# Performance work log

Measured on AMD Instinct MI355X. Metric: run time of the kernel, lower is better.

The kernel has to match this reference:

```python
import jax, jax.numpy as jnp
import numpy as np

CONF_TH = 0.9
FRACTION = 0.66
IGNORE_INDEX = 255
LAMBDA = 1.0


def setup_inputs() -> dict:
    key = jax.random.key(0)
    pred = jax.random.normal(key, (4, 19, 512, 1024), dtype=jnp.float32)
    return {"pred": pred}


def _image_mask(max_prob, pseudo, num_classes):
    # max_prob, pseudo: [N] flattened per-image. Replicates the torch per-class
    # loop: keep the top floor(count_c * FRACTION) pixels of each class c by
    # max_prob. Equivalent to: within-class descending rank < k_c.
    n = max_prob.shape[0]
    # sort by (class asc, prob desc); last key in lexsort is primary
    order = jnp.lexsort((-max_prob, pseudo))
    counts = jnp.bincount(pseudo, length=num_classes)  # [C]
    starts = jnp.concatenate([jnp.zeros(1, counts.dtype), jnp.cumsum(counts)[:-1]])
    rank_sorted = jnp.arange(n, dtype=counts.dtype) - starts[pseudo[order]]
    rank = jnp.zeros(n, counts.dtype).at[order].set(rank_sorted)
    k = jnp.floor(counts.astype(jnp.float32) * FRACTION).astype(counts.dtype)  # int(count*frac)
    mask_topk = rank < k[pseudo]
    mask_prob = max_prob > CONF_TH
    return mask_prob | mask_topk


def reference(pred):
    B, C, H, W = pred.shape
    logp = jax.nn.log_softmax(pred, axis=1)           # [B,C,H,W]
    prob = jnp.exp(logp)
    pseudo = jnp.argmax(pred, axis=1)                 # [B,H,W] (detached in torch; int here)
    max_prob = jnp.max(prob, axis=1)                  # [B,H,W]
    N = H * W
    mask = jax.vmap(lambda m, p: _image_mask(m, p, C))(
        max_prob.reshape(B, N), pseudo.reshape(B, N)
    ).reshape(B, H, W)
    target = jnp.where(mask, pseudo, IGNORE_INDEX)
    valid = target != IGNORE_INDEX
    tsafe = jnp.where(valid, target, 0)
    nll = -jnp.take_along_axis(logp, tsafe[:, None], axis=1)[:, 0]  # [B,H,W]
    # F.cross_entropy(..., reduction='none') gives 0 at ignored pixels; .mean()
    # divides by the TOTAL number of pixels (including ignored ones).
    loss = jnp.where(valid, nll, 0.0).mean() * LAMBDA
    return loss
```

## Files before the change

### kernel.cpp

```cpp
#include <hip/hip_runtime.h>
#include <math.h>

#define BB 4
#define CC 19
#define HH 512
#define WW 1024
#define NPIX (HH * WW)
#define NB 80
#define CONF_BIN 72
#define FRACTION_F 0.66f
#define ROW (CC * NB)
#define NROW (BB * CC)

#define NBLK1 512
#define BPI (NBLK1 / BB)
#define PPB (NPIX / BPI)
#define T1 512


static __device__ __forceinline__ float comp(float4 v, int j) {
    return (j == 0) ? v.x : (j == 1) ? v.y : (j == 2) ? v.z : v.w;
}

__global__ __launch_bounds__(T1, 4) void st_pass1(const float* __restrict__ pred,
                                                  int* __restrict__ cntPart,
                                                  float* __restrict__ snlPart,
                                                  float* __restrict__ out) {
    __shared__ int   hcnt[ROW];
    __shared__ float hsnl[ROW];
    int tid = threadIdx.x;
    if (blockIdx.x == 0 && tid == 0) out[0] = 0.f;
    for (int i = tid; i < ROW; i += T1) { hcnt[i] = 0; hsnl[i] = 0.f; }
    __syncthreads();

    int blk = blockIdx.x;
    int b   = blk >> 7;
    int seg = blk & (BPI - 1);
    const float* bp0 = pred + (size_t)b * CC * NPIX + (size_t)seg * PPB + tid * 4;
    const float* bp1 = bp0 + T1 * 4;

    float4 va[5], vb[5], vc[5], vd[4];
    float m[4], s[4]; int arg[4];

#define LOAD5(DST, BP, C0)                                            \
        _Pragma("unroll")                                             \
        for (int i = 0; i < 5; ++i)                                   \
            DST[i] = *(const float4*)((BP) + (size_t)(C0 + i) * NPIX);
#define LOAD4(DST, BP, C0)                                            \
        _Pragma("unroll")                                             \
        for (int i = 0; i < 4; ++i)                                   \
            DST[i] = *(const float4*)((BP) + (size_t)(C0 + i) * NPIX);
#define FENCE asm volatile("" ::: "memory")
#define INIT4(VA)                                                     \
        _Pragma("unroll")                                             \
        for (int j = 0; j < 4; ++j) { m[j] = comp(VA[0], j); s[j] = 1.f; arg[j] = 0; }
#define PROC(VA, NCH, CBASE, START)                                   \
        _Pragma("unroll")                                             \
        for (int i = START; i < NCH; ++i) {                           \
            _Pragma("unroll")                                         \
            for (int j = 0; j < 4; ++j) {                             \
                float x  = comp(VA[i], j);                            \
                float nm = fmaxf(m[j], x);                            \
                s[j] = s[j] * __expf(m[j] - nm) + __expf(x - nm);     \
                arg[j] = (x > m[j]) ? (CBASE + i) : arg[j];           \
                m[j] = nm;                                            \
            }                                                         \
        }
#define FINAL()                                                       \
        _Pragma("unroll")                                             \
        for (int j = 0; j < 4; ++j) {                                 \
            float prob = 1.f / s[j];                                  \
            float nll  = __logf(s[j]);                                \
            int bin = min((int)(prob * (float)NB), NB - 1);           \
            int idx = arg[j] * NB + bin;                              \
            atomicAdd(&hcnt[idx], 1);                                 \
            atomicAdd(&hsnl[idx], nll);                               \
        }

    LOAD5(va, bp0, 0); LOAD5(vb, bp0, 5); FENCE;
    INIT4(va)
    PROC(va, 5, 0, 1)
    LOAD5(vc, bp0, 10); FENCE;
    PROC(vb, 5, 5, 0)
    LOAD4(vd, bp0, 15); FENCE;
    PROC(vc, 5, 10, 0)
    LOAD5(va, bp1, 0); FENCE;
    PROC(vd, 4, 15, 0)
    FINAL()
    LOAD5(vb, bp1, 5); FENCE;
    INIT4(va)
    PROC(va, 5, 0, 1)
    LOAD5(vc, bp1, 10); FENCE;
    PROC(vb, 5, 5, 0)
    LOAD4(vd, bp1, 15); FENCE;
    PROC(vc, 5, 10, 0)
    PROC(vd, 4, 15, 0)
    FINAL()
#undef LOAD5
#undef LOAD4
#undef FENCE
#undef INIT4
#undef PROC
#undef FINAL
    __syncthreads();

    int*   cp = cntPart + (size_t)blk * ROW;
    float* sp = snlPart + (size_t)blk * ROW;
    for (int i = tid; i < ROW; i += T1) { cp[i] = hcnt[i]; sp[i] = hsnl[i]; }
}

__global__ __launch_bounds__(384) void st_pass2(const int* __restrict__ cntPart,
                                                const float* __restrict__ snlPart,
                                                float* __restrict__ out) {
    __shared__ int   pcnt[4][NB];
    __shared__ float psnl[4][NB];
    __shared__ int   scnt[NB];
    __shared__ float ssnl[NB];
    int r = blockIdx.x;
    int b = r / CC, c = r - b * CC;
    int tid = threadIdx.x;

    if (tid < 4 * NB) {
        int q   = tid / NB;
        int bin = tid - q * NB;
        size_t off = (size_t)(b * BPI + q * 32) * ROW + (size_t)(c * NB + bin);
        int cs0 = 0, cs1 = 0; float ss0 = 0.f, ss1 = 0.f;
        #pragma unroll 8
        for (int p = 0; p < 32; p += 2) {
            cs0 += cntPart[off + (size_t)p * ROW];
            cs1 += cntPart[off + (size_t)(p + 1) * ROW];
            ss0 += snlPart[off + (size_t)p * ROW];
            ss1 += snlPart[off + (size_t)(p + 1) * ROW];
        }
        pcnt[q][bin] = cs0 + cs1;
        psnl[q][bin] = ss0 + ss1;
    }
    __syncthreads();
    if (tid < NB) {
        scnt[tid] = (pcnt[0][tid] + pcnt[1][tid]) + (pcnt[2][tid] + pcnt[3][tid]);
        ssnl[tid] = (psnl[0][tid] + psnl[1][tid]) + (psnl[2][tid] + psnl[3][tid]);
    }
    __syncthreads();

    if (tid == 0) {
        int count = 0;
        #pragma unroll 8
        for (int i = 0; i < NB; ++i) count += scnt[i];
        float conf = 0.f;
        #pragma unroll 8
        for (int i = CONF_BIN; i < NB; ++i) conf += ssnl[i];
        int k = (int)floorf((float)count * FRACTION_F);
        float sel;
        if (k == 0) {
            sel = conf;
        } else {
            int cum = 0;
            float csum = 0.f;
            int bin = NB - 1;
            int hh = 0;
            for (; bin >= 0; --bin) {
                hh = scnt[bin];
                if (cum + hh >= k) break;
                cum += hh;
                csum += ssnl[bin];
            }
            if (bin < 0) {
                sel = csum;
            } else if (bin >= CONF_BIN) {
                sel = conf;
            } else {
                float avg = ssnl[bin] / (float)max(hh, 1);
                sel = csum + (float)(k - cum) * avg;
            }
        }
        atomicAdd(out, sel * (1.0f / (float)(BB * (size_t)NPIX)));
    }
}

extern "C" void kernel_launch(void* const* d_in, const int* in_sizes, int n_in,
                              void* d_out, int out_size, void* d_ws, size_t ws_size,
                              hipStream_t stream) {
    const float* pred = (const float*)d_in[0];
    float* out = (float*)d_out;

    char* ws = (char*)d_ws;
    int*   cntPart = (int*)ws;
    float* snlPart = (float*)(ws + (size_t)NBLK1 * ROW * sizeof(int));

    st_pass1<<<NBLK1, T1, 0, stream>>>(pred, cntPart, snlPart, out);
    st_pass2<<<NROW, 384, 0, stream>>>(cntPart, snlPart, out);
}
```

Before: 41.63 us.

## Stream pass1 input through triple-buffered LDS using direct global-to-LDS loads

Pass 1 now uses half as many blocks. Each block loops over 512-pixel chunks that are loaded with global_load_lds into a three-deep shared-memory ring, with manual vmcnt waits and barriers between stages. Each thread then handles one pixel per chunk with scalar softmax, instead of four pixels held in register float4 arrays. The goal is deeper memory-level parallelism and fewer registers, but it adds two barriers per chunk, about 117KB of LDS per block (limiting occupancy), and the pass-2 reduction is resized to match the new partial count.

```diff
diff --git a/kernel.cpp b/kernel.cpp
--- a/kernel.cpp
+++ b/kernel.cpp
@@ -3,105 +3,93 @@
 
 #define BB 4
 #define CC 19
-#define HH 512
-#define WW 1024
-#define NPIX (HH * WW)
+#define NPIX (512 * 1024)
 #define NB 80
 #define CONF_BIN 72
 #define FRACTION_F 0.66f
 #define ROW (CC * NB)
 #define NROW (BB * CC)
 
-#define NBLK1 512
+#define NBLK1 256
 #define BPI (NBLK1 / BB)
-#define PPB (NPIX / BPI)
+#define SEG (NPIX / BPI)
+#define CHUNK 512
+#define NCHUNK (SEG / CHUNK)
 #define T1 512
+#define BUFELE (CHUNK * CC)
+#define NBUF 3
 
 
-static __device__ __forceinline__ float comp(float4 v, int j) {
-    return (j == 0) ? v.x : (j == 1) ? v.y : (j == 2) ? v.z : v.w;
+__device__ __forceinline__ void gload16(const float* g, float* l) {
+    __builtin_amdgcn_global_load_lds(
+        (const __attribute__((address_space(1))) unsigned int*)g,
+        (__attribute__((address_space(3))) unsigned int*)l, 16, 0, 0);
 }
 
-__global__ __launch_bounds__(T1, 4) void st_pass1(const float* __restrict__ pred,
-                                                  int* __restrict__ cntPart,
-                                                  float* __restrict__ snlPart,
-                                                  float* __restrict__ out) {
+#define BAR() asm volatile("s_barrier" ::: "memory")
+
+__global__ __launch_bounds__(T1) void st_pass1(const float* __restrict__ pred,
+                                               int* __restrict__ cntPart,
+                                               float* __restrict__ snlPart,
+                                               float* __restrict__ out) {
+    __shared__ float sbuf[NBUF * BUFELE];
     __shared__ int   hcnt[ROW];
     __shared__ float hsnl[ROW];
-    int tid = threadIdx.x;
-    if (blockIdx.x == 0 && tid == 0) out[0] = 0.f;
+
+    int tid  = threadIdx.x;
+    int lane = tid & 63;
+    int wid  = tid >> 6;
+    int blk  = blockIdx.x;
+    int b    = blk >> 6;
+    int seg  = blk & (BPI - 1);
+
+    if (blk == 0 && tid == 0) out[0] = 0.f;
     for (int i = tid; i < ROW; i += T1) { hcnt[i] = 0; hsnl[i] = 0.f; }
     __syncthreads();
 
-    int blk = blockIdx.x;
-    int b   = blk >> 7;
-    int seg = blk & (BPI - 1);
-    const float* bp0 = pred + (size_t)b * CC * NPIX + (size_t)seg * PPB + tid * 4;
-    const float* bp1 = bp0 + T1 * 4;
+    const float* gbase = pred + (size_t)b * CC * NPIX + (size_t)seg * SEG;
 
-    float4 va[5], vb[5], vc[5], vd[4];
-    float m[4], s[4]; int arg[4];
+    auto issue = [&](int t, int bufsel) {
+        const float* gc = gbase + (size_t)t * CHUNK + lane * 4;
+        float* lb = sbuf + bufsel * BUFELE;
+        for (int i = wid; i < 2 * CC; i += 8) {
+            int c = i >> 1, h = i & 1;
+            gload16(gc + (size_t)c * NPIX + h * 256, lb + c * CHUNK + h * 256);
+        }
+    };
 
-#define LOAD5(DST, BP, C0)                                            \
-        _Pragma("unroll")                                             \
-        for (int i = 0; i < 5; ++i)                                   \
-            DST[i] = *(const float4*)((BP) + (size_t)(C0 + i) * NPIX);
-#define LOAD4(DST, BP, C0)                                            \
-        _Pragma("unroll")                                             \
-        for (int i = 0; i < 4; ++i)                                   \
-            DST[i] = *(const float4*)((BP) + (size_t)(C0 + i) * NPIX);
-#define FENCE asm volatile("" ::: "memory")
-#define INIT4(VA)                                                     \
-        _Pragma("unroll")                                             \
-        for (int j = 0; j < 4; ++j) { m[j] = comp(VA[0], j); s[j] = 1.f; arg[j] = 0; }
-#define PROC(VA, NCH, CBASE, START)                                   \
-        _Pragma("unroll")                                             \
-        for (int i = START; i < NCH; ++i) {                           \
-            _Pragma("unroll")                                         \
-            for (int j = 0; j < 4; ++j) {                             \
-                float x  = comp(VA[i], j);                            \
-                float nm = fmaxf(m[j], x);                            \
-                s[j] = s[j] * __expf(m[j] - nm) + __expf(x - nm);     \
-                arg[j] = (x > m[j]) ? (CBASE + i) : arg[j];           \
-                m[j] = nm;                                            \
-            }                                                         \
+    issue(0, 0);
+    issue(1, 1);
+
+    for (int t = 0; t < NCHUNK; ++t) {
+        if (t + 2 < NCHUNK) issue(t + 2, (t + 2) % 3);
+
+        if (t < NCHUNK - 2)       asm volatile("s_waitcnt vmcnt(8)" ::: "memory");
+        else if (t == NCHUNK - 2) asm volatile("s_waitcnt vmcnt(4)" ::: "memory");
+        else                      asm volatile("s_waitcnt vmcnt(0)" ::: "memory");
+        BAR();
+
+        const float* lb = sbuf + (t % 3) * BUFELE;
+        float m = lb[tid];
+        float s = 1.f;
+        int arg = 0;
+        #pragma unroll
+        for (int c = 1; c < CC; ++c) {
+            float x  = lb[c * CHUNK + tid];
+            float nm = fmaxf(m, x);
+            s = s * __expf(m - nm) + __expf(x - nm);
+            arg = (x > m) ? c : arg;
+            m = nm;
         }
-#define FINAL()                                                       \
-        _Pragma("unroll")                                             \
-        for (int j = 0; j < 4; ++j) {                                 \
-            float prob = 1.f / s[j];                                  \
-            float nll  = __logf(s[j]);                                \
-            int bin = min((int)(prob * (float)NB), NB - 1);           \
-            int idx = arg[j] * NB + bin;                              \
-            atomicAdd(&hcnt[idx], 1);                                 \
-            atomicAdd(&hsnl[idx], nll);                               \
-        }
+        float prob = 1.f / s;
+        float nll  = __logf(s);
+        int bin = min((int)(prob * (float)NB), NB - 1);
+        int idx = arg * NB + bin;
+        atomicAdd(&hcnt[idx], 1);
+        atomicAdd(&hsnl[idx], nll);
 
-    LOAD5(va, bp0, 0); LOAD5(vb, bp0, 5); FENCE;
-    INIT4(va)
-    PROC(va, 5, 0, 1)
-    LOAD5(vc, bp0, 10); FENCE;
-    PROC(vb, 5, 5, 0)
-    LOAD4(vd, bp0, 15); FENCE;
-    PROC(vc, 5, 10, 0)
-    LOAD5(va, bp1, 0); FENCE;
-    PROC(vd, 4, 15, 0)
-    FINAL()
-    LOAD5(vb, bp1, 5); FENCE;
-    INIT4(va)
-    PROC(va, 5, 0, 1)
-    LOAD5(vc, bp1, 10); FENCE;
-    PROC(vb, 5, 5, 0)
-    LOAD4(vd, bp1, 15); FENCE;
-    PROC(vc, 5, 10, 0)
-    PROC(vd, 4, 15, 0)
-    FINAL()
-#undef LOAD5
-#undef LOAD4
-#undef FENCE
-#undef INIT4
-#undef PROC
-#undef FINAL
+        BAR();
+    }
     __syncthreads();
 
     int*   cp = cntPart + (size_t)blk * ROW;
@@ -109,7 +97,7 @@
     for (int i = tid; i < ROW; i += T1) { cp[i] = hcnt[i]; sp[i] = hsnl[i]; }
 }
 
-__global__ __launch_bounds__(384) void st_pass2(const int* __restrict__ cntPart,
+__global__ __launch_bounds__(320) void st_pass2(const int* __restrict__ cntPart,
                                                 const float* __restrict__ snlPart,
                                                 float* __restrict__ out) {
     __shared__ int   pcnt[4][NB];
@@ -120,13 +108,13 @@
     int b = r / CC, c = r - b * CC;
     int tid = threadIdx.x;
 
-    if (tid < 4 * NB) {
+    {
         int q   = tid / NB;
         int bin = tid - q * NB;
-        size_t off = (size_t)(b * BPI + q * 32) * ROW + (size_t)(c * NB + bin);
+        size_t off = (size_t)(b * BPI + q * 16) * ROW + (size_t)(c * NB + bin);
         int cs0 = 0, cs1 = 0; float ss0 = 0.f, ss1 = 0.f;
         #pragma unroll 8
-        for (int p = 0; p < 32; p += 2) {
+        for (int p = 0; p < 16; p += 2) {
             cs0 += cntPart[off + (size_t)p * ROW];
             cs1 += cntPart[off + (size_t)(p + 1) * ROW];
             ss0 += snlPart[off + (size_t)p * ROW];
@@ -188,5 +176,5 @@
     float* snlPart = (float*)(ws + (size_t)NBLK1 * ROW * sizeof(int));
 
     st_pass1<<<NBLK1, T1, 0, stream>>>(pred, cntPart, snlPart, out);
-    st_pass2<<<NROW, 384, 0, stream>>>(cntPart, snlPart, out);
+    st_pass2<<<NROW, 320, 0, stream>>>(cntPart, snlPart, out);
 }
```

Measured after the change: 48.78 us. +17.2%, slower.
